# Performance work log

Measured on AMD Instinct MI355X. Metric: run time of the kernel, lower is better.

Reference implementation:

```python
import jax, jax.numpy as jnp
import numpy as np

INF8 = 255
H, D = 8, 64  # num_heads, head dim (hidden=512)
G = 1         # num_global_node


def setup_inputs() -> dict:
    key = jax.random.key(0)
    ks = jax.random.split(key, 12)
    B, N, HID = 8, 1023, 512
    S = N + G
    inp = {
        'q': jax.random.normal(ks[0], (B, S, HID), jnp.float32),
        'k': jax.random.normal(ks[1], (B, S, HID), jnp.float32),
        'v': jax.random.normal(ks[2], (B, S, HID), jnp.float32),
        'attn_bias': jax.random.randint(ks[3], (B, N, N, 1), 0, 255).astype(jnp.int32),
        'Wq': 0.02 * jax.random.normal(ks[4], (HID, HID), jnp.float32),
        'bq': jnp.zeros((HID,), jnp.float32),
        'Wk': 0.02 * jax.random.normal(ks[5], (HID, HID), jnp.float32),
        'bk': jnp.zeros((HID,), jnp.float32),
        'Wv': 0.02 * jax.random.normal(ks[6], (HID, HID), jnp.float32),
        'bv': jnp.zeros((HID,), jnp.float32),
        'Wo': 0.02 * jax.random.normal(ks[7], (HID, HID), jnp.float32),
        'bo': jnp.zeros((HID,), jnp.float32),
        'bias_table': 0.02 * jax.random.normal(ks[8], (INF8 + 1, H), jnp.float32),
        'vbias': 0.02 * jax.random.normal(ks[9], (G, H), jnp.float32),
    }
    return inp


def _structural_bias(attn_bias, bias_table, vbias):
    # attn_bias: [B, N, N, 1] int -> [B, H, N+G, N+G] float
    ab = attn_bias[..., 0]                      # [B,N,N]
    B, N, _ = ab.shape
    bias = bias_table[ab]                       # [B,N,N,H]
    mask = ab == INF8
    bias = jnp.where(mask[..., None], -jnp.inf, bias)
    row = jnp.broadcast_to(vbias[None, :, None, :], (B, G, N, bias.shape[-1]))
    bias = jnp.concatenate([bias, row], axis=1)             # [B,N+G,N,H]
    col = jnp.broadcast_to(vbias[None, None, :, :], (B, N + G, G, bias.shape[-1]))
    bias = jnp.concatenate([bias, col], axis=2)             # [B,N+G,N+G,H]
    return bias.transpose(0, 3, 1, 2)                       # [B,H,S,S]


def reference(q, k, v, attn_bias, Wq, bq, Wk, bk, Wv, bv, Wo, bo, bias_table, vbias):
    B, S, HID = q.shape
    scale = D ** -0.5
    qh = (q @ Wq.T + bq).reshape(B, S, H, D)
    kh = (k @ Wk.T + bk).reshape(B, S, H, D)
    vh = (v @ Wv.T + bv).reshape(B, S, H, D)
    scores = jnp.einsum('bshd,bthd->bhst', qh * scale, kh)  # [B,H,S,S]
    scores = scores + _structural_bias(attn_bias, bias_table, vbias)
    p = jax.nn.softmax(scores, axis=-1)
    # dropout is identity in eval mode
    ctx = jnp.einsum('bhst,bthd->bshd', p, vh).reshape(B, S, HID)
    return ctx @ Wo.T + bo
```

## Files before the change

### kernel.cpp

```cpp
#include <hip/hip_runtime.h>
#include <hip/hip_bf16.h>


typedef __attribute__((ext_vector_type(8)))  __bf16 bf16x8;
typedef __attribute__((ext_vector_type(16))) float  f32x16;

__device__ inline f32x16 zero16(){
  f32x16 z;
  #pragma unroll
  for (int i=0;i<16;i++) z[i] = 0.0f;
  return z;
}

__device__ inline unsigned short f2bf(float x){
  unsigned u = __float_as_uint(x);
  u += 0x7fffu + ((u>>16)&1u);
  return (unsigned short)(u>>16);
}
__device__ inline unsigned f2bf_pair(float a, float b){
  unsigned ua = __float_as_uint(a); ua += 0x7fffu + ((ua>>16)&1u);
  unsigned ub = __float_as_uint(b); ub += 0x7fffu + ((ub>>16)&1u);
  return (ua>>16) | (ub & 0xffff0000u);
}
__device__ inline unsigned comb2(unsigned a, unsigned b, float rn){
  const float a0 = __uint_as_float(a<<16), a1 = __uint_as_float(a & 0xffff0000u);
  const float b0 = __uint_as_float(b<<16), b1 = __uint_as_float(b & 0xffff0000u);
  return f2bf_pair((a0+b0)*rn, (a1+b1)*rn);
}

__device__ inline void bar_lgkm(){
  asm volatile("s_waitcnt lgkmcnt(0)" ::: "memory");
  __builtin_amdgcn_s_barrier();
}

__global__ __launch_bounds__(256)
void ab_transpose(const int* ab, unsigned char* abT)
{
  __shared__ int tl[64*65];
  const int k  = blockIdx.x;
  const int b  = k >> 8;
  const int ti = k & 255;
  const int t0 = (ti & 15) << 6, q0 = (ti >> 4) << 6;
  const int c  = threadIdx.x & 63, r0 = threadIdx.x >> 6;
  #pragma unroll
  for (int rp = 0; rp < 16; ++rp){
    const int r = r0 + rp*4;
    const int q = q0 + r, t = t0 + c;
    int v = 255;
    if (q < 1023 && t < 1023) v = ab[((size_t)b*1023 + q)*1023 + t];
    tl[r*65 + c] = v;
  }
  __syncthreads();
  unsigned char* dst = abT + ((size_t)b << 20);
  #pragma unroll
  for (int rp = 0; rp < 16; ++rp){
    const int r = r0 + rp*4;
    dst[(size_t)(t0 + r)*1024 + q0 + c] = (unsigned char)tl[c*65 + r];
  }
}

__global__ __launch_bounds__(256)
void qkv_proj(const float* xq, const float* xk, const float* xv,
              const float* Wq, const float* Wk, const float* Wv,
              const float* bq, const float* bk, const float* bv,
              unsigned short* qh, unsigned short* kh, unsigned short* vht2,
              float scaleq)
{
  __shared__ unsigned short lda[2][128*40];
  __shared__ unsigned short ldb[2][128*40];
  const int bid = blockIdx.x;
  const int sel = bid >> 8;
  const int t   = bid & 255;
  const float *RA, *RB, *bias;
  int r0, c0;
  if (sel == 0){ RA = xq; RB = Wq; bias = bq; r0 = (t&63)*128; c0 = (t>>6)*128; }
  else if (sel == 1){ RA = xk; RB = Wk; bias = bk; r0 = (t&63)*128; c0 = (t>>6)*128; }
  else { RA = Wv; RB = xv; bias = bv; r0 = (t&3)*128; c0 = (t>>2)*128; }

  const int tid  = threadIdx.x;
  const int w    = tid>>6, lane = tid&63, lo = lane&31, hi = lane>>5;
  const int wr   = (w>>1)*64, wc = (w&1)*64;
  const int arow = tid>>1, kb = (tid&1)*16;

  f32x16 acc[2][2];
  #pragma unroll
  for (int i=0;i<2;i++)
    #pragma unroll
    for (int j=0;j<2;j++) acc[i][j] = zero16();

  float4 ra[4], rb4[4];

  {
    const float4* p = (const float4*)(RA + (r0+arow)*512 + kb);
    ra[0]=p[0]; ra[1]=p[1]; ra[2]=p[2]; ra[3]=p[3];
    const float4* pq = (const float4*)(RB + (c0+arow)*512 + kb);
    rb4[0]=pq[0]; rb4[1]=pq[1]; rb4[2]=pq[2]; rb4[3]=pq[3];
  }
  {
    uint4 w0, w1;
    w0.x = f2bf_pair(ra[0].x, ra[0].y); w0.y = f2bf_pair(ra[0].z, ra[0].w);
    w0.z = f2bf_pair(ra[1].x, ra[1].y); w0.w = f2bf_pair(ra[1].z, ra[1].w);
    w1.x = f2bf_pair(ra[2].x, ra[2].y); w1.y = f2bf_pair(ra[2].z, ra[2].w);
    w1.z = f2bf_pair(ra[3].x, ra[3].y); w1.w = f2bf_pair(ra[3].z, ra[3].w);
    uint4* pa = (uint4*)&lda[0][arow*40 + kb];
    pa[0] = w0; pa[1] = w1;
    uint4 v0, v1;
    v0.x = f2bf_pair(rb4[0].x, rb4[0].y); v0.y = f2bf_pair(rb4[0].z, rb4[0].w);
    v0.z = f2bf_pair(rb4[1].x, rb4[1].y); v0.w = f2bf_pair(rb4[1].z, rb4[1].w);
    v1.x = f2bf_pair(rb4[2].x, rb4[2].y); v1.y = f2bf_pair(rb4[2].z, rb4[2].w);
    v1.z = f2bf_pair(rb4[3].x, rb4[3].y); v1.w = f2bf_pair(rb4[3].z, rb4[3].w);
    uint4* pb = (uint4*)&ldb[0][arow*40 + kb];
    pb[0] = v0; pb[1] = v1;
  }
  {
    const float4* p = (const float4*)(RA + (r0+arow)*512 + 32 + kb);
    ra[0]=p[0]; ra[1]=p[1]; ra[2]=p[2]; ra[3]=p[3];
    const float4* pq = (const float4*)(RB + (c0+arow)*512 + 32 + kb);
    rb4[0]=pq[0]; rb4[1]=pq[1]; rb4[2]=pq[2]; rb4[3]=pq[3];
  }
  bar_lgkm();

  for (int ks=0; ks<16; ++ks){
    const int cur = ks & 1;
    if (ks < 15){
      uint4 w0, w1;
      w0.x = f2bf_pair(ra[0].x, ra[0].y); w0.y = f2bf_pair(ra[0].z, ra[0].w);
      w0.z = f2bf_pair(ra[1].x, ra[1].y); w0.w = f2bf_pair(ra[1].z, ra[1].w);
      w1.x = f2bf_pair(ra[2].x, ra[2].y); w1.y = f2bf_pair(ra[2].z, ra[2].w);
      w1.z = f2bf_pair(ra[3].x, ra[3].y); w1.w = f2bf_pair(ra[3].z, ra[3].w);
      uint4* pa = (uint4*)&lda[cur^1][arow*40 + kb];
      pa[0] = w0; pa[1] = w1;
      uint4 v0, v1;
      v0.x = f2bf_pair(rb4[0].x, rb4[0].y); v0.y = f2bf_pair(rb4[0].z, rb4[0].w);
      v0.z = f2bf_pair(rb4[1].x, rb4[1].y); v0.w = f2bf_pair(rb4[1].z, rb4[1].w);
      v1.x = f2bf_pair(rb4[2].x, rb4[2].y); v1.y = f2bf_pair(rb4[2].z, rb4[2].w);
      v1.z = f2bf_pair(rb4[3].x, rb4[3].y); v1.w = f2bf_pair(rb4[3].z, rb4[3].w);
      uint4* pb = (uint4*)&ldb[cur^1][arow*40 + kb];
      pb[0] = v0; pb[1] = v1;
    }
    if (ks < 14){
      const int k0 = (ks+2)*32;
      const float4* p = (const float4*)(RA + (r0+arow)*512 + k0 + kb);
      ra[0]=p[0]; ra[1]=p[1]; ra[2]=p[2]; ra[3]=p[3];
      const float4* pq = (const float4*)(RB + (c0+arow)*512 + k0 + kb);
      rb4[0]=pq[0]; rb4[1]=pq[1]; rb4[2]=pq[2]; rb4[3]=pq[3];
    }
    #pragma unroll
    for (int kf=0; kf<2; ++kf){
      bf16x8 af0 = *(const bf16x8*)&lda[cur][(wr+lo)*40    + kf*16 + hi*8];
      bf16x8 af1 = *(const bf16x8*)&lda[cur][(wr+32+lo)*40 + kf*16 + hi*8];
      bf16x8 bg0 = *(const bf16x8*)&ldb[cur][(wc+lo)*40    + kf*16 + hi*8];
      bf16x8 bg1 = *(const bf16x8*)&ldb[cur][(wc+32+lo)*40 + kf*16 + hi*8];
      acc[0][0] = __builtin_amdgcn_mfma_f32_32x32x16_bf16(af0, bg0, acc[0][0], 0,0,0);
      acc[0][1] = __builtin_amdgcn_mfma_f32_32x32x16_bf16(af0, bg1, acc[0][1], 0,0,0);
      acc[1][0] = __builtin_amdgcn_mfma_f32_32x32x16_bf16(af1, bg0, acc[1][0], 0,0,0);
      acc[1][1] = __builtin_amdgcn_mfma_f32_32x32x16_bf16(af1, bg1, acc[1][1], 0,0,0);
    }
    bar_lgkm();
  }

  #pragma unroll
  for (int mi=0;mi<2;mi++){
    #pragma unroll
    for (int ni=0;ni<2;ni++){
      #pragma unroll
      for (int r=0;r<16;r++){
        const int rl = wr + mi*32 + (r&3) + 8*(r>>2) + 4*hi;
        const int cl = wc + ni*32 + lo;
        const int rg = r0 + rl, cg = c0 + cl;
        float v = acc[mi][ni][r];
        if (sel == 0){
          v = (v + bias[cg]) * scaleq;
          const int bb = rg>>10, s = rg&1023, h = cg>>6, d = cg&63;
          qh[(((bb*8+h)*1024)+s)*64 + d] = f2bf(v);
        } else if (sel == 1){
          v = v + bias[cg];
          const int bb = rg>>10, s = rg&1023, h = cg>>6, d = cg&63;
          kh[(((bb*8+h)*1024)+s)*64 + d] = f2bf(v);
        } else {
          v = v + bias[rg];
          const int h = rg>>6, d = rg&63, bb = cg>>10, s = cg&1023;
          vht2[(((size_t)(bb*8+h)*32 + (s>>5))*64 + d)*32 + (s&31)] = f2bf(v);
        }
      }
    }
  }
}

__global__ __launch_bounds__(256)
void out_proj(const unsigned short* ctx0, const unsigned short* ctx1,
              const float* lsump, const float* Wo, const float* bo, float* OUT)
{
  __shared__ unsigned short lda[128*40];
  __shared__ unsigned short ldb[128*40];
  const int tid  = threadIdx.x;
  const int r0   = blockIdx.x*128, c0 = blockIdx.y*128;
  const int w    = tid>>6, lane = tid&63, lo = lane&31, hi = lane>>5;
  const int wr   = (w>>1)*64, wc = (w&1)*64;
  const int arow = tid>>1, kb = (tid&1)*16;
  const int rgs  = r0 + arow, bb = rgs>>10, ss = rgs&1023;
  const float* lb0 = lsump + (size_t)(bb*8)*1024 + ss;
  const float* lb1 = lsump + (size_t)((8+bb)*8)*1024 + ss;

  f32x16 acc[2][2];
  #pragma unroll
  for (int i=0;i<2;i++)
    #pragma unroll
    for (int j=0;j<2;j++) acc[i][j] = zero16();

  uint4 ra0[2], ra1[2];
  float4 rb4[4];
  float l0, l1;

  {
    const uint4* p0 = (const uint4*)(ctx0 + rgs*512 + kb);
    ra0[0]=p0[0]; ra0[1]=p0[1];
    const uint4* p1 = (const uint4*)(ctx1 + rgs*512 + kb);
    ra1[0]=p1[0]; ra1[1]=p1[1];
    const int h = kb>>6;
    l0 = lb0[h*1024]; l1 = lb1[h*1024];
    const float4* pq = (const float4*)(Wo + (c0+arow)*512 + kb);
    rb4[0]=pq[0]; rb4[1]=pq[1]; rb4[2]=pq[2]; rb4[3]=pq[3];
  }

  for (int ks=0; ks<16; ++ks){
    bar_lgkm();
    {
      const float rn = __builtin_amdgcn_rcpf(l0 + l1);
      uint4 w0, w1;
      w0.x = comb2(ra0[0].x, ra1[0].x, rn); w0.y = comb2(ra0[0].y, ra1[0].y, rn);
      w0.z = comb2(ra0[0].z, ra1[0].z, rn); w0.w = comb2(ra0[0].w, ra1[0].w, rn);
      w1.x = comb2(ra0[1].x, ra1[1].x, rn); w1.y = comb2(ra0[1].y, ra1[1].y, rn);
      w1.z = comb2(ra0[1].z, ra1[1].z, rn); w1.w = comb2(ra0[1].w, ra1[1].w, rn);
      uint4* pa = (uint4*)&lda[arow*40 + kb];
      pa[0] = w0; pa[1] = w1;
      uint4 v0, v1;
      v0.x = f2bf_pair(rb4[0].x, rb4[0].y); v0.y = f2bf_pair(rb4[0].z, rb4[0].w);
      v0.z = f2bf_pair(rb4[1].x, rb4[1].y); v0.w = f2bf_pair(rb4[1].z, rb4[1].w);
      v1.x = f2bf_pair(rb4[2].x, rb4[2].y); v1.y = f2bf_pair(rb4[2].z, rb4[2].w);
      v1.z = f2bf_pair(rb4[3].x, rb4[3].y); v1.w = f2bf_pair(rb4[3].z, rb4[3].w);
      uint4* pb = (uint4*)&ldb[arow*40 + kb];
      pb[0] = v0; pb[1] = v1;
    }
    if (ks < 15){
      const int k0 = (ks+1)*32;
      const uint4* p0 = (const uint4*)(ctx0 + rgs*512 + k0 + kb);
      ra0[0]=p0[0]; ra0[1]=p0[1];
      const uint4* p1 = (const uint4*)(ctx1 + rgs*512 + k0 + kb);
      ra1[0]=p1[0]; ra1[1]=p1[1];
      const int h = (k0+kb)>>6;
      l0 = lb0[h*1024]; l1 = lb1[h*1024];
      const float4* pq = (const float4*)(Wo + (c0+arow)*512 + k0 + kb);
      rb4[0]=pq[0]; rb4[1]=pq[1]; rb4[2]=pq[2]; rb4[3]=pq[3];
    }
    bar_lgkm();
    #pragma unroll
    for (int kf=0; kf<2; ++kf){
      bf16x8 af0 = *(const bf16x8*)&lda[(wr+lo)*40    + kf*16 + hi*8];
      bf16x8 af1 = *(const bf16x8*)&lda[(wr+32+lo)*40 + kf*16 + hi*8];
      bf16x8 bg0 = *(const bf16x8*)&ldb[(wc+lo)*40    + kf*16 + hi*8];
      bf16x8 bg1 = *(const bf16x8*)&ldb[(wc+32+lo)*40 + kf*16 + hi*8];
      acc[0][0] = __builtin_amdgcn_mfma_f32_32x32x16_bf16(af0, bg0, acc[0][0], 0,0,0);
      acc[0][1] = __builtin_amdgcn_mfma_f32_32x32x16_bf16(af0, bg1, acc[0][1], 0,0,0);
      acc[1][0] = __builtin_amdgcn_mfma_f32_32x32x16_bf16(af1, bg0, acc[1][0], 0,0,0);
      acc[1][1] = __builtin_amdgcn_mfma_f32_32x32x16_bf16(af1, bg1, acc[1][1], 0,0,0);
    }
  }

  #pragma unroll
  for (int mi=0;mi<2;mi++){
    #pragma unroll
    for (int ni=0;ni<2;ni++){
      #pragma unroll
      for (int r=0;r<16;r++){
        const int rl = wr + mi*32 + (r&3) + 8*(r>>2) + 4*hi;
        const int cl = wc + ni*32 + lo;
        const int rg = r0 + rl, cg = c0 + cl;
        OUT[rg*512 + cg] = acc[mi][ni][r] + bo[cg];
      }
    }
  }
}

__global__ __launch_bounds__(256)
void attn_fused(const unsigned short* qh, const unsigned short* kh,
                const unsigned short* vht2, const unsigned char* abT,
                const float* bias_table, const float* vbias,
                unsigned short* ctxp, float* lsump)
{
  __shared__ float tbl[256];
  __shared__ unsigned short kls[2][32*72];
  __shared__ unsigned short vls[2][64*40];
  __shared__ unsigned char  abls[2][32*136];

  const int tid = threadIdx.x;
  const int m   = blockIdx.x;
  const int b   = m & 7;
  const int r   = m >> 3;
  const int h   = r & 7;
  const int ts  = (r >> 3) & 1;
  const int sg  = r >> 4;
  const int tb  = ts*512;
  const int q0  = sg*128;

  {
    const int i = tid;
    float v = (i < 255) ? bias_table[i*8 + h] : vbias[h];
    tbl[i] = v * 1.4426950408889634f;
  }

  const int w = tid>>6, lane = tid&63, lo = lane&31, hi = lane>>5;
  const bool hib = (hi != 0);
  const int s0 = q0 + w*32;

  const unsigned short* qbase  = qh   + (size_t)(b*8+h)*65536;
  const unsigned short* kbase  = kh   + (size_t)(b*8+h)*65536 + (size_t)tb*64;
  const unsigned short* vbase  = vht2 + ((size_t)(b*8+h)*32 + (tb>>5))*2048;
  const unsigned char*  abbase = abT  + ((size_t)b<<20) + q0;

  bf16x8 qf[4];
  #pragma unroll
  for (int kf=0; kf<4; ++kf)
    qf[kf] = *(const bf16x8*)&qbase[(s0+lo)*64 + kf*16 + hi*8];

  f32x16 accv[2]; accv[0] = zero16(); accv[1] = zero16();
  float lsum = 0.0f;

  const int kdst = (tid>>3)*72  + (tid&7)*8;
  const int vdst = (tid>>2)*40  + (tid&3)*8;
  const int adst = (tid>>3)*136 + (tid&7)*16;

  uint4 krg, vrg, ar0;
  krg = *(const uint4*)&kbase[tid*8];
  vrg = *(const uint4*)&vbase[tid*8];
  ar0 = *(const uint4*)&abbase[(size_t)(tb + (tid>>3))*1024 + (tid&7)*16];
  *(uint4*)&kls[0][kdst]  = krg;
  *(uint4*)&vls[0][vdst]  = vrg;
  *(uint4*)&abls[0][adst] = ar0;
  krg = *(const uint4*)&kbase[32*64 + tid*8];
  vrg = *(const uint4*)&vbase[2048 + tid*8];
  ar0 = *(const uint4*)&abbase[(size_t)(tb + 32 + (tid>>3))*1024 + (tid&7)*16];
  bar_lgkm();

  for (int tt=0; tt<512; tt+=32){
    const int cur = (tt>>5) & 1;
    *(uint4*)&kls[cur^1][kdst]  = krg;
    *(uint4*)&vls[cur^1][vdst]  = vrg;
    *(uint4*)&abls[cur^1][adst] = ar0;
    {
      const int tn = (tt+64)&511;
      krg = *(const uint4*)&kbase[tn*64 + tid*8];
      vrg = *(const uint4*)&vbase[(tn>>5)*2048 + tid*8];
      ar0 = *(const uint4*)&abbase[(size_t)(tb + tn + (tid>>3))*1024 + (tid&7)*16];
    }

    f32x16 sc = zero16();
    #pragma unroll
    for (int kf=0; kf<4; ++kf){
      bf16x8 kfr = *(const bf16x8*)&kls[cur][lo*72 + kf*16 + hi*8];
      sc = __builtin_amdgcn_mfma_f32_32x32x16_bf16(kfr, qf[kf], sc, 0,0,0);
    }

    unsigned d[4][2];
    float ls = 0.0f;
    #pragma unroll
    for (int g=0; g<4; ++g){
      float p[4];
      #pragma unroll
      for (int u=0; u<4; ++u){
        const int crow = u + 8*g + 4*hi;
        const int idx  = abls[cur][crow*136 + w*32 + lo];
        p[u] = __builtin_amdgcn_exp2f(sc[4*g+u] + tbl[idx]);
        ls  += p[u];
      }
      d[g][0] = f2bf_pair(p[0], p[1]);
      d[g][1] = f2bf_pair(p[2], p[3]);
    }
    lsum += ls;

    unsigned x[4][2];
    #pragma unroll
    for (int g=0; g<4; ++g){
      x[g][0] = __shfl_xor(d[g][0], 32, 64);
      x[g][1] = __shfl_xor(d[g][1], 32, 64);
    }

    #pragma unroll
    for (int c2=0; c2<2; ++c2){
      union { unsigned u[4]; bf16x8 v; } pc;
      pc.u[0] = hib ? x[2*c2+1][0] : d[2*c2][0];
      pc.u[1] = hib ? x[2*c2+1][1] : d[2*c2][1];
      pc.u[2] = hib ? d[2*c2+1][0] : x[2*c2][0];
      pc.u[3] = hib ? d[2*c2+1][1] : x[2*c2][1];
      bf16x8 vf0 = *(const bf16x8*)&vls[cur][(     lo)*40 + c2*16 + hi*8];
      bf16x8 vf1 = *(const bf16x8*)&vls[cur][(32 + lo)*40 + c2*16 + hi*8];
      accv[0] = __builtin_amdgcn_mfma_f32_32x32x16_bf16(pc.v, vf0, accv[0], 0,0,0);
      accv[1] = __builtin_amdgcn_mfma_f32_32x32x16_bf16(pc.v, vf1, accv[1], 0,0,0);
    }
    bar_lgkm();
  }

  lsum += __shfl_xor(lsum, 32, 64);

  unsigned short* cbase = ctxp + (size_t)ts*4194304;
  #pragma unroll
  for (int dc=0; dc<2; ++dc){
    #pragma unroll
    for (int r2=0;r2<16;r2++){
      const int rq = (r2&3) + 8*(r2>>2) + 4*hi;
      cbase[((size_t)b*1024 + s0 + rq)*512 + h*64 + dc*32 + lo] = f2bf(accv[dc][r2]);
    }
  }
  if (hi == 0){
    lsump[((size_t)(ts*8 + b)*8 + h)*1024 + s0 + lo] = lsum;
  }
}

extern "C" void kernel_launch(void* const* d_in, const int* in_sizes, int n_in,
                              void* d_out, int out_size, void* d_ws, size_t ws_size,
                              hipStream_t stream)
{
  const float* q    = (const float*)d_in[0];
  const float* k    = (const float*)d_in[1];
  const float* v    = (const float*)d_in[2];
  const int*   ab   = (const int*)  d_in[3];
  const float* Wq   = (const float*)d_in[4];
  const float* bq   = (const float*)d_in[5];
  const float* Wk   = (const float*)d_in[6];
  const float* bk   = (const float*)d_in[7];
  const float* Wv   = (const float*)d_in[8];
  const float* bv   = (const float*)d_in[9];
  const float* Wo   = (const float*)d_in[10];
  const float* bo   = (const float*)d_in[11];
  const float* btab = (const float*)d_in[12];
  const float* vbia = (const float*)d_in[13];

  char* ws = (char*)d_ws;
  unsigned short* qh   = (unsigned short*)(ws);
  unsigned short* kh   = (unsigned short*)(ws + ((size_t) 8<<20));
  unsigned short* vht2 = (unsigned short*)(ws + ((size_t)16<<20));
  unsigned short* ctxp = (unsigned short*)(ws + ((size_t)24<<20));
  float*          lsmp = (float*)         (ws + ((size_t)40<<20));
  unsigned char*  abT  = (unsigned char*) (ws + ((size_t)41<<20));

  const float SCALE_Q = 0.125f * 1.4426950408889634f;

  qkv_proj<<<768, 256, 0, stream>>>(q, k, v, Wq, Wk, Wv, bq, bk, bv,
                                    qh, kh, vht2, SCALE_Q);
  ab_transpose<<<2048, 256, 0, stream>>>(ab, abT);
  attn_fused<<<1024, 256, 0, stream>>>(qh, kh, vht2, abT, btab, vbia,
                                       ctxp, lsmp);
  out_proj<<<dim3(64,4), 256, 0, stream>>>(ctxp, ctxp + (size_t)4194304,
                                           lsmp, Wo, bo, (float*)d_out);
}
```

Measured before the change: 121.3 us.

## Replace attn-bias transpose with row-major uint8 pack and packed LDS reads

Drops the tiled LDS transpose of the int32 attention-bias matrix. The prep kernel now packs each row straight into uint8, four values per 32-bit store. The attention kernel stages query-major bias tiles, so each lane reads four consecutive indices with one 32-bit LDS load and extracts them by shifting, instead of four byte loads. This simplifies the prep kernel and cuts LDS load instructions in the inner loop. In exchange, the prep kernel's global reads are strided per thread (each thread reads 4 consecutive ints), and the global loads in the attention kernel change pattern.

```diff
diff --git a/kernel.cpp b/kernel.cpp
--- a/kernel.cpp
+++ b/kernel.cpp
@@ -34,28 +34,27 @@
 }
 
 __global__ __launch_bounds__(256)
-void ab_transpose(const int* ab, unsigned char* abT)
+void ab_u8(const int* ab, unsigned char* ab8)
 {
-  __shared__ int tl[64*65];
-  const int k  = blockIdx.x;
-  const int b  = k >> 8;
-  const int ti = k & 255;
-  const int t0 = (ti & 15) << 6, q0 = (ti >> 4) << 6;
-  const int c  = threadIdx.x & 63, r0 = threadIdx.x >> 6;
-  #pragma unroll
-  for (int rp = 0; rp < 16; ++rp){
-    const int r = r0 + rp*4;
-    const int q = q0 + r, t = t0 + c;
-    int v = 255;
-    if (q < 1023 && t < 1023) v = ab[((size_t)b*1023 + q)*1023 + t];
-    tl[r*65 + c] = v;
-  }
-  __syncthreads();
-  unsigned char* dst = abT + ((size_t)b << 20);
-  #pragma unroll
-  for (int rp = 0; rp < 16; ++rp){
-    const int r = r0 + rp*4;
-    dst[(size_t)(t0 + r)*1024 + q0 + c] = (unsigned char)tl[c*65 + r];
+  const int k   = blockIdx.x;
+  const int b   = k >> 8;
+  const int q   = ((k & 255) << 2) + (threadIdx.x >> 6);
+  const int j   = threadIdx.x & 63;
+  const bool qok = (q < 1023);
+  const int* rowp = ab + ((size_t)b*1023 + q)*1023;
+  unsigned char* outp = ab8 + ((size_t)b << 20) + (size_t)q*1024;
+  #pragma unroll
+  for (int i = 0; i < 4; ++i){
+    const int t0 = (j + 64*i)*4;
+    unsigned o = 0;
+    #pragma unroll
+    for (int c = 0; c < 4; ++c){
+      const int t = t0 + c;
+      int v = 255;
+      if (qok && t < 1023) v = rowp[t];
+      o |= ((unsigned)v & 255u) << (8*c);
+    }
+    *(unsigned*)(outp + t0) = o;
   }
 }
 
@@ -284,14 +283,14 @@
 
 __global__ __launch_bounds__(256)
 void attn_fused(const unsigned short* qh, const unsigned short* kh,
-                const unsigned short* vht2, const unsigned char* abT,
+                const unsigned short* vht2, const unsigned char* ab8,
                 const float* bias_table, const float* vbias,
                 unsigned short* ctxp, float* lsump)
 {
   __shared__ float tbl[256];
   __shared__ unsigned short kls[2][32*72];
   __shared__ unsigned short vls[2][64*40];
-  __shared__ unsigned char  abls[2][32*136];
+  __shared__ unsigned char  abls[2][128*36];
 
   const int tid = threadIdx.x;
   const int m   = blockIdx.x;
@@ -316,7 +315,7 @@
   const unsigned short* qbase  = qh   + (size_t)(b*8+h)*65536;
   const unsigned short* kbase  = kh   + (size_t)(b*8+h)*65536 + (size_t)tb*64;
   const unsigned short* vbase  = vht2 + ((size_t)(b*8+h)*32 + (tb>>5))*2048;
-  const unsigned char*  abbase = abT  + ((size_t)b<<20) + q0;
+  const unsigned char*  abbase = ab8  + ((size_t)b<<20);
 
   bf16x8 qf[4];
   #pragma unroll
@@ -328,18 +327,19 @@
 
   const int kdst = (tid>>3)*72  + (tid&7)*8;
   const int vdst = (tid>>2)*40  + (tid&3)*8;
-  const int adst = (tid>>3)*136 + (tid&7)*16;
+  const int adst = (tid>>1)*36  + (tid&1)*16;
+  const size_t asrc = (size_t)(q0 + (tid>>1))*1024 + (tid&1)*16;
 
   uint4 krg, vrg, ar0;
   krg = *(const uint4*)&kbase[tid*8];
   vrg = *(const uint4*)&vbase[tid*8];
-  ar0 = *(const uint4*)&abbase[(size_t)(tb + (tid>>3))*1024 + (tid&7)*16];
+  ar0 = *(const uint4*)&abbase[asrc + tb];
   *(uint4*)&kls[0][kdst]  = krg;
   *(uint4*)&vls[0][vdst]  = vrg;
   *(uint4*)&abls[0][adst] = ar0;
   krg = *(const uint4*)&kbase[32*64 + tid*8];
   vrg = *(const uint4*)&vbase[2048 + tid*8];
-  ar0 = *(const uint4*)&abbase[(size_t)(tb + 32 + (tid>>3))*1024 + (tid&7)*16];
+  ar0 = *(const uint4*)&abbase[asrc + tb + 32];
   bar_lgkm();
 
   for (int tt=0; tt<512; tt+=32){
@@ -351,7 +351,7 @@
       const int tn = (tt+64)&511;
       krg = *(const uint4*)&kbase[tn*64 + tid*8];
       vrg = *(const uint4*)&vbase[(tn>>5)*2048 + tid*8];
-      ar0 = *(const uint4*)&abbase[(size_t)(tb + tn + (tid>>3))*1024 + (tid&7)*16];
+      ar0 = *(const uint4*)&abbase[asrc + tb + tn];
     }
 
     f32x16 sc = zero16();
@@ -361,15 +361,16 @@
       sc = __builtin_amdgcn_mfma_f32_32x32x16_bf16(kfr, qf[kf], sc, 0,0,0);
     }
 
+    const unsigned char* abrow = &abls[cur][(w*32 + lo)*36];
     unsigned d[4][2];
     float ls = 0.0f;
     #pragma unroll
     for (int g=0; g<4; ++g){
+      const unsigned v4 = *(const unsigned*)(abrow + 8*g + 4*hi);
       float p[4];
       #pragma unroll
       for (int u=0; u<4; ++u){
-        const int crow = u + 8*g + 4*hi;
-        const int idx  = abls[cur][crow*136 + w*32 + lo];
+        const int idx = (v4 >> (8*u)) & 255;
         p[u] = __builtin_amdgcn_exp2f(sc[4*g+u] + tbl[idx]);
         ls  += p[u];
       }
@@ -441,14 +442,14 @@
   unsigned short* vht2 = (unsigned short*)(ws + ((size_t)16<<20));
   unsigned short* ctxp = (unsigned short*)(ws + ((size_t)24<<20));
   float*          lsmp = (float*)         (ws + ((size_t)40<<20));
-  unsigned char*  abT  = (unsigned char*) (ws + ((size_t)41<<20));
+  unsigned char*  ab8  = (unsigned char*) (ws + ((size_t)41<<20));
 
   const float SCALE_Q = 0.125f * 1.4426950408889634f;
 
   qkv_proj<<<768, 256, 0, stream>>>(q, k, v, Wq, Wk, Wv, bq, bk, bv,
                                     qh, kh, vht2, SCALE_Q);
-  ab_transpose<<<2048, 256, 0, stream>>>(ab, abT);
-  attn_fused<<<1024, 256, 0, stream>>>(qh, kh, vht2, abT, btab, vbia,
+  ab_u8<<<2048, 256, 0, stream>>>(ab, ab8);
+  attn_fused<<<1024, 256, 0, stream>>>(qh, kh, vht2, ab8, btab, vbia,
                                        ctxp, lsmp);
   out_proj<<<dim3(64,4), 256, 0, stream>>>(ctxp, ctxp + (size_t)4194304,
                                            lsmp, Wo, bo, (float*)d_out);
```

Result: no change. 121.1 us (-0.2%).
